# Optimization experiments

Measured on AMD Instinct MI355X. Metric: run time of the kernel, lower is better.

## Reference

```python
import jax, jax.numpy as jnp
import numpy as np

B, S, D, H = 2, 2048, 1024, 16
HD = D // H  # head dim = 64
NEG = -1e9


def setup_inputs() -> dict:
    key = jax.random.key(0)
    ks = jax.random.split(key, 8)
    x = jax.random.normal(ks[0], (B, S, D), dtype=jnp.float32)
    mask = jax.random.randint(ks[1], (B, 1, S, S), 0, 2).astype(bool)
    s = 1.0 / np.sqrt(D)
    Wq = jax.random.normal(ks[2], (D, D), dtype=jnp.float32) * s
    bq = jax.random.normal(ks[3], (D,), dtype=jnp.float32) * 0.01
    Wk = jax.random.normal(ks[4], (D, D), dtype=jnp.float32) * s
    bk = jax.random.normal(ks[5], (D,), dtype=jnp.float32) * 0.01
    Wv = jax.random.normal(ks[6], (D, D), dtype=jnp.float32) * s
    bv = jax.random.normal(ks[7], (D,), dtype=jnp.float32) * 0.01
    return {"x": x, "mask": mask, "Wq": Wq, "bq": bq, "Wk": Wk, "bk": bk, "Wv": Wv, "bv": bv}


def reference(x, mask, Wq, bq, Wk, bk, Wv, bv):
    b, s, d = x.shape
    # QKV projections (torch nn.Linear: y = x @ W.T + b)
    q = (x @ Wq.T + bq).reshape(b, s, H, HD).transpose(0, 2, 1, 3)  # [B,H,S,HD]
    k = (x @ Wk.T + bk).reshape(b, s, H, HD).transpose(0, 2, 1, 3)
    v = (x @ Wv.T + bv).reshape(b, s, H, HD).transpose(0, 2, 1, 3)
    # NOTE: original scales by sqrt(hidden_state), not sqrt(head_dim)
    scale = 1.0 / jnp.sqrt(jnp.asarray(d, dtype=x.dtype))
    weight = jnp.einsum('bhqd,bhkd->bhqk', q, k) * scale  # [B,H,S,S]
    weight = jnp.where(mask, jnp.asarray(NEG, dtype=x.dtype), weight)
    score = jax.nn.softmax(weight, axis=-1)
    out = jnp.einsum('bhqk,bhkd->bhqd', score, v)  # [B,H,S,HD]
    return out.transpose(0, 2, 1, 3).reshape(b, s, d)
```

## Files before the change

### kernel.cpp

```cpp
#include <hip/hip_runtime.h>
#include <hip/hip_bf16.h>

typedef __bf16 bf16x8 __attribute__((ext_vector_type(8)));
typedef float f32x4 __attribute__((ext_vector_type(4)));

#define NB 2
#define NS 2048
#define ND 1024
#define NH 16
#define NHD 64

__device__ __forceinline__ unsigned short f2b(float f) {
    union { __hip_bfloat16 h; unsigned short u; } c;
    c.h = __float2bfloat16(f);
    return c.u;
}

__device__ __forceinline__ void gl_lds16(const unsigned short* g, unsigned short* l) {
    __builtin_amdgcn_global_load_lds(
        (const __attribute__((address_space(1))) unsigned int*)g,
        (__attribute__((address_space(3))) unsigned int*)l, 16, 0, 0);
}

__global__ __launch_bounds__(256) void to_bf16_all(
    const float* __restrict__ x,  const float* __restrict__ wq,
    const float* __restrict__ wk, const float* __restrict__ wv,
    unsigned short* __restrict__ xb,  unsigned short* __restrict__ wqb,
    unsigned short* __restrict__ wkb, unsigned short* __restrict__ wvb)
{
    const size_t TX = (size_t)NB * NS * ND / 8;
    const size_t TW = (size_t)ND * ND / 8;
    size_t gid = (size_t)blockIdx.x * 256 + threadIdx.x;
    const float* src; unsigned short* dst; size_t off;
    if (gid < TX)               { src = x;  dst = xb;  off = gid * 8; }
    else if (gid < TX + TW)     { src = wq; dst = wqb; off = (gid - TX) * 8; }
    else if (gid < TX + 2 * TW) { src = wk; dst = wkb; off = (gid - TX - TW) * 8; }
    else                        { src = wv; dst = wvb; off = (gid - TX - 2 * TW) * 8; }
    float4 a = *(const float4*)(src + off);
    float4 b = *(const float4*)(src + off + 4);
    alignas(16) unsigned short t[8];
    t[0] = f2b(a.x); t[1] = f2b(a.y); t[2] = f2b(a.z); t[3] = f2b(a.w);
    t[4] = f2b(b.x); t[5] = f2b(b.y); t[6] = f2b(b.z); t[7] = f2b(b.w);
    *(uint4*)(dst + off) = *(const uint4*)t;
}

__global__ void detect_mask(const unsigned* __restrict__ m, int* __restrict__ flag) {
    __shared__ int bad;
    if (threadIdx.x == 0) bad = 0;
    __syncthreads();
    int mybad = 0;
    for (int i = threadIdx.x; i < 8192; i += 256) {
        unsigned w = m[i];
        if (w != 0u && w != 1u && w != 0x3F800000u) mybad = 1;
    }
    if (mybad) bad = 1;
    __syncthreads();
    if (threadIdx.x == 0) *flag = bad ? 0 : 1;
}

__global__ __launch_bounds__(256) void pack_mask(
    const void* __restrict__ mask, const int* __restrict__ mflag,
    unsigned long long* __restrict__ mbits)
{
    const int wave = threadIdx.x >> 6;
    const int lane = threadIdx.x & 63;
    const size_t w = (size_t)blockIdx.x * 4 + wave;
    const size_t e = w * 64 + lane;
    int v;
    if (*mflag) v = (((const unsigned*)mask)[e] != 0u);
    else        v = (((const unsigned char*)mask)[e] != 0);
    unsigned long long bits = __ballot(v);
    if (lane == 0) mbits[w] = bits;
}

__global__ __launch_bounds__(256) void qkv_gemm(
    const unsigned short* __restrict__ xb,
    const unsigned short* __restrict__ Wqb, const float* __restrict__ bq,
    const unsigned short* __restrict__ Wkb, const float* __restrict__ bk,
    const unsigned short* __restrict__ Wvb, const float* __restrict__ bv,
    unsigned short* __restrict__ Qb, unsigned short* __restrict__ Kb,
    unsigned short* __restrict__ Vtb)
{
    __shared__ alignas(16) unsigned short Alds[128 * 64];
    __shared__ alignas(16) unsigned short Blds[128 * 64];

    const int tid  = threadIdx.x;
    const int wave = tid >> 6;
    const int lane = tid & 63;
    const int z    = blockIdx.z;

    const unsigned short* W = (z == 0) ? Wqb : (z == 1) ? Wkb : Wvb;
    const float* bias       = (z == 0) ? bq  : (z == 1) ? bk  : bv;

    const int m0 = blockIdx.x * 128;
    const int n0 = blockIdx.y * 128;
    const int wr = (wave >> 1) * 64;
    const int wc = (wave & 1) * 64;

    int soff[4];
    #pragma unroll
    for (int i = 0; i < 4; i++) {
        const int r = i * 32 + (tid >> 3);
        soff[i] = r * ND + (((tid & 7) ^ (r & 7)) * 8);
    }

    const unsigned short* xsrc = xb + (size_t)m0 * ND;
    const unsigned short* wsrc = W  + (size_t)n0 * ND;

    const int lg = lane >> 4;
    const int ll = lane & 15;
    const int xr7 = ll & 7;

    f32x4 acc[4][4] = {};

    for (int kt = 0; kt < ND; kt += 64) {
        if (kt != 0) __syncthreads();
        #pragma unroll
        for (int i = 0; i < 4; i++) {
            gl_lds16(xsrc + kt + soff[i], Alds + i * 2048 + wave * 512);
            gl_lds16(wsrc + kt + soff[i], Blds + i * 2048 + wave * 512);
        }
        __syncthreads();

        #pragma unroll
        for (int kk = 0; kk < 2; kk++) {
            const int segb = ((kk * 4 + lg) ^ xr7) * 16;
            bf16x8 af[4], bfr[4];
            #pragma unroll
            for (int m = 0; m < 4; m++)
                af[m] = *(const bf16x8*)((const char*)Alds
                         + (wr + m * 16 + ll) * 128 + segb);
            #pragma unroll
            for (int n = 0; n < 4; n++)
                bfr[n] = *(const bf16x8*)((const char*)Blds
                         + (wc + n * 16 + ll) * 128 + segb);

            #pragma unroll
            for (int m = 0; m < 4; m++)
                #pragma unroll
                for (int n = 0; n < 4; n++)
                    acc[m][n] = __builtin_amdgcn_mfma_f32_16x16x32_bf16(
                        af[m], bfr[n], acc[m][n], 0, 0, 0);
        }
    }

    const float oscale = (z == 0) ? 0.03125f : 1.0f;
    #pragma unroll
    for (int n = 0; n < 4; n++) {
        const int j  = n0 + wc + n * 16 + ll;
        const float bj = bias[j];
        const int hh = j >> 6;
        const int hd = j & 63;
        #pragma unroll
        for (int m = 0; m < 4; m++) {
            #pragma unroll
            for (int r = 0; r < 4; r++) {
                const int i  = m0 + wr + m * 16 + lg * 4 + r;
                const int bb = i >> 11;
                const int sI = i & 2047;
                const unsigned short o = f2b((acc[m][n][r] + bj) * oscale);
                if (z == 2) {
                    Vtb[((size_t)(bb * NH + hh) * NHD + hd) * NS + sI] = o;
                } else {
                    const size_t idx = ((size_t)(bb * NH + hh) * NS + sI) * NHD + hd;
                    if (z == 0) Qb[idx] = o; else Kb[idx] = o;
                }
            }
        }
    }
}

__global__ __launch_bounds__(512, 4) void attn_kernel(
    const unsigned short* __restrict__ Qb, const unsigned short* __restrict__ Kb,
    const unsigned short* __restrict__ Vtb,
    const unsigned long long* __restrict__ mbits, float* __restrict__ out)
{
    __shared__ alignas(16) unsigned short Kt[64 * 64];
    __shared__ alignas(16) unsigned short Vt[64 * 64];
    __shared__ alignas(16) unsigned short Plds[8][16][72];

    const int tid  = threadIdx.x;
    const int wave = tid >> 6;
    const int lane = tid & 63;

    const int wg   = blockIdx.x;
    const int xcd  = wg & 7;
    const int slot = wg >> 3;
    const int hb   = xcd * 4 + (slot >> 4);
    const int qblk = slot & 15;
    const int h = hb & (NH - 1);
    const int b = hb >> 4;
    const int q0 = qblk * 128 + wave * 16;

    const unsigned short* Qp = Qb  + (size_t)(b * NH + h) * NS * NHD;
    const unsigned short* Kp = Kb  + (size_t)(b * NH + h) * NS * NHD;
    const unsigned short* Vp = Vtb + (size_t)(b * NH + h) * NHD * NS;
    const unsigned long long* mrow = mbits + (size_t)b * NS * (NS / 64);

    const int lg = lane >> 4;
    const int ll = lane & 15;

    const int rw = wave * 8 + (lane >> 3);
    const int sg = (lane & 7) ^ (rw & 7);
    const size_t ksoff = (size_t)rw * NHD + sg * 8;
    const size_t vsoff = (size_t)rw * NS  + sg * 8;
    unsigned short* ldsK = Kt + wave * 512;
    unsigned short* ldsV = Vt + wave * 512;

    const int xr7 = ll & 7;
    const int ka0 = ll * 128 + ((lg)     ^ xr7) * 16;
    const int ka1 = ll * 128 + ((lg + 4) ^ xr7) * 16;

    const int kcol = lg * 8;
    const bf16x8 qf0 = *(const bf16x8*)&Qp[(q0 + ll) * NHD + kcol];
    const bf16x8 qf1 = *(const bf16x8*)&Qp[(q0 + ll) * NHD + 32 + kcol];

    f32x4 O0 = {}, O1 = {}, O2 = {}, O3 = {};
    float mrun = -3.0e38f;
    float lrun = 0.f;

    unsigned long long mwc = mrow[(size_t)(q0 + ll) * (NS / 64)];

    for (int t = 0; t < 32; t++) {
        const int kb = t * 64;
        if (t != 0) __syncthreads();
        gl_lds16(Kp + (size_t)kb * NHD + ksoff, ldsK);
        gl_lds16(Vp + kb + vsoff, ldsV);
        const int tn = (t + 1 < 32) ? t + 1 : 0;
        const unsigned long long mwn = mrow[(size_t)(q0 + ll) * (NS / 64) + tn];
        __syncthreads();

        f32x4 s0 = {}, s1 = {}, s2 = {}, s3 = {};
        {
            const bf16x8 k00 = *(const bf16x8*)((const char*)Kt + 0 * 2048 + ka0);
            const bf16x8 k10 = *(const bf16x8*)((const char*)Kt + 1 * 2048 + ka0);
            const bf16x8 k20 = *(const bf16x8*)((const char*)Kt + 2 * 2048 + ka0);
            const bf16x8 k30 = *(const bf16x8*)((const char*)Kt + 3 * 2048 + ka0);
            s0 = __builtin_amdgcn_mfma_f32_16x16x32_bf16(k00, qf0, s0, 0, 0, 0);
            s1 = __builtin_amdgcn_mfma_f32_16x16x32_bf16(k10, qf0, s1, 0, 0, 0);
            s2 = __builtin_amdgcn_mfma_f32_16x16x32_bf16(k20, qf0, s2, 0, 0, 0);
            s3 = __builtin_amdgcn_mfma_f32_16x16x32_bf16(k30, qf0, s3, 0, 0, 0);
            const bf16x8 k01 = *(const bf16x8*)((const char*)Kt + 0 * 2048 + ka1);
            const bf16x8 k11 = *(const bf16x8*)((const char*)Kt + 1 * 2048 + ka1);
            const bf16x8 k21 = *(const bf16x8*)((const char*)Kt + 2 * 2048 + ka1);
            const bf16x8 k31 = *(const bf16x8*)((const char*)Kt + 3 * 2048 + ka1);
            s0 = __builtin_amdgcn_mfma_f32_16x16x32_bf16(k01, qf1, s0, 0, 0, 0);
            s1 = __builtin_amdgcn_mfma_f32_16x16x32_bf16(k11, qf1, s1, 0, 0, 0);
            s2 = __builtin_amdgcn_mfma_f32_16x16x32_bf16(k21, qf1, s2, 0, 0, 0);
            s3 = __builtin_amdgcn_mfma_f32_16x16x32_bf16(k31, qf1, s3, 0, 0, 0);
        }

        const unsigned long long mws = mwc >> (lg * 4);
        float sv[16];
        #pragma unroll
        for (int tt = 0; tt < 4; tt++) {
            const f32x4 st = (tt == 0) ? s0 : (tt == 1) ? s1 : (tt == 2) ? s2 : s3;
            #pragma unroll
            for (int r = 0; r < 4; r++)
                sv[tt * 4 + r] = ((mws >> (16 * tt + r)) & 1ull) ? -1e9f : st[r];
        }

        float m01 = fmaxf(fmaxf(sv[0], sv[1]), fmaxf(sv[2], sv[3]));
        float m23 = fmaxf(fmaxf(sv[4], sv[5]), fmaxf(sv[6], sv[7]));
        float m45 = fmaxf(fmaxf(sv[8], sv[9]), fmaxf(sv[10], sv[11]));
        float m67 = fmaxf(fmaxf(sv[12], sv[13]), fmaxf(sv[14], sv[15]));
        float mt = fmaxf(fmaxf(m01, m23), fmaxf(m45, m67));
        mt = fmaxf(mt, __shfl_xor(mt, 16));
        mt = fmaxf(mt, __shfl_xor(mt, 32));

        if (!__all(mt <= mrun + 8.0f)) {
            const float mnew  = fmaxf(mrun, mt);
            const float alpha = __expf(mrun - mnew);
            mrun = mnew;
            lrun *= alpha;
            #pragma unroll
            for (int r = 0; r < 4; r++) {
                const float ar = __shfl(alpha, lg * 4 + r);
                O0[r] *= ar; O1[r] *= ar; O2[r] *= ar; O3[r] *= ar;
            }
        }

        float rs = 0.f;
        #pragma unroll
        for (int tt = 0; tt < 4; tt++) {
            const float p0 = __expf(sv[tt * 4 + 0] - mrun);
            const float p1 = __expf(sv[tt * 4 + 1] - mrun);
            const float p2 = __expf(sv[tt * 4 + 2] - mrun);
            const float p3 = __expf(sv[tt * 4 + 3] - mrun);
            rs += (p0 + p1) + (p2 + p3);
            uint2 w;
            w.x = (unsigned)f2b(p0) | ((unsigned)f2b(p1) << 16);
            w.y = (unsigned)f2b(p2) | ((unsigned)f2b(p3) << 16);
            *(uint2*)&Plds[wave][ll][tt * 16 + lg * 4] = w;
        }
        rs += __shfl_xor(rs, 16);
        rs += __shfl_xor(rs, 32);
        lrun += rs;

        const bf16x8 pa0 = *(const bf16x8*)&Plds[wave][ll][kcol];
        const bf16x8 pa1 = *(const bf16x8*)&Plds[wave][ll][32 + kcol];
        {
            const bf16x8 v00 = *(const bf16x8*)((const char*)Vt + 0 * 2048 + ka0);
            const bf16x8 v10 = *(const bf16x8*)((const char*)Vt + 1 * 2048 + ka0);
            const bf16x8 v20 = *(const bf16x8*)((const char*)Vt + 2 * 2048 + ka0);
            const bf16x8 v30 = *(const bf16x8*)((const char*)Vt + 3 * 2048 + ka0);
            O0 = __builtin_amdgcn_mfma_f32_16x16x32_bf16(pa0, v00, O0, 0, 0, 0);
            O1 = __builtin_amdgcn_mfma_f32_16x16x32_bf16(pa0, v10, O1, 0, 0, 0);
            O2 = __builtin_amdgcn_mfma_f32_16x16x32_bf16(pa0, v20, O2, 0, 0, 0);
            O3 = __builtin_amdgcn_mfma_f32_16x16x32_bf16(pa0, v30, O3, 0, 0, 0);
            const bf16x8 v01 = *(const bf16x8*)((const char*)Vt + 0 * 2048 + ka1);
            const bf16x8 v11 = *(const bf16x8*)((const char*)Vt + 1 * 2048 + ka1);
            const bf16x8 v21 = *(const bf16x8*)((const char*)Vt + 2 * 2048 + ka1);
            const bf16x8 v31 = *(const bf16x8*)((const char*)Vt + 3 * 2048 + ka1);
            O0 = __builtin_amdgcn_mfma_f32_16x16x32_bf16(pa1, v01, O0, 0, 0, 0);
            O1 = __builtin_amdgcn_mfma_f32_16x16x32_bf16(pa1, v11, O1, 0, 0, 0);
            O2 = __builtin_amdgcn_mfma_f32_16x16x32_bf16(pa1, v21, O2, 0, 0, 0);
            O3 = __builtin_amdgcn_mfma_f32_16x16x32_bf16(pa1, v31, O3, 0, 0, 0);
        }
        mwc = mwn;
    }

    #pragma unroll
    for (int r = 0; r < 4; r++) {
        const int q = q0 + lg * 4 + r;
        const float inv = 1.0f / __shfl(lrun, lg * 4 + r);
        float* op = out + (size_t)(b * NS + q) * ND + h * NHD;
        op[0 * 16 + ll] = O0[r] * inv;
        op[1 * 16 + ll] = O1[r] * inv;
        op[2 * 16 + ll] = O2[r] * inv;
        op[3 * 16 + ll] = O3[r] * inv;
    }
}

extern "C" void kernel_launch(void* const* d_in, const int* in_sizes, int n_in,
                              void* d_out, int out_size, void* d_ws, size_t ws_size,
                              hipStream_t stream)
{
    const float* x  = (const float*)d_in[0];
    const void* mask = d_in[1];
    const float* Wq = (const float*)d_in[2];
    const float* bq = (const float*)d_in[3];
    const float* Wk = (const float*)d_in[4];
    const float* bk = (const float*)d_in[5];
    const float* Wv = (const float*)d_in[6];
    const float* bv = (const float*)d_in[7];
    float* out = (float*)d_out;

    const size_t szX = (size_t)NB * NS * ND;
    const size_t szW = (size_t)ND * ND;
    const size_t szQ = (size_t)NB * NH * NS * NHD;

    int* mflag = (int*)d_ws;
    unsigned short* xb  = (unsigned short*)((char*)d_ws + 256);
    unsigned short* Wqb = xb  + szX;
    unsigned short* Wkb = Wqb + szW;
    unsigned short* Wvb = Wkb + szW;
    unsigned short* Qb  = Wvb + szW;
    unsigned short* Kb  = Qb + szQ;
    unsigned short* Vtb = Kb + szQ;
    unsigned long long* mbits = (unsigned long long*)(Vtb + szQ);

    dim3 blk(256);
    const int cvtBlocks = (int)((szX + 3 * szW) / 8 / 256);
    to_bf16_all<<<dim3(cvtBlocks), blk, 0, stream>>>(
        x, Wq, Wk, Wv, xb, Wqb, Wkb, Wvb);

    detect_mask<<<dim3(1), blk, 0, stream>>>((const unsigned*)mask, mflag);
    const int words = NB * NS * NS / 64;
    pack_mask<<<dim3(words / 4), blk, 0, stream>>>(mask, mflag, mbits);

    dim3 g1(32, 8, 3);
    qkv_gemm<<<g1, blk, 0, stream>>>(xb, Wqb, bq, Wkb, bk, Wvb, bv, Qb, Kb, Vtb);

    attn_kernel<<<dim3(512), dim3(512), 0, stream>>>(Qb, Kb, Vtb, mbits, out);
}
```

Measured before the change: 234.4 us.

## Double-buffer K/V tiles, stage QKV epilogue through LDS, use exp2 softmax

The attention kernel now double-buffers the K and V LDS tiles. The next tile's global-to-LDS load is issued before computing on the current one, with a single barrier per iteration, so load latency overlaps MFMA work. The projection epilogue for Q and K is staged through LDS scratch so global stores become 16-byte vectors, and V transposed stores are packed four at a time. The Q scale is folded with log2(e) so softmax can use exp2f instead of expf. The cost is doubled K/V LDS, which may reduce occupancy, plus an extra barrier in the GEMM epilogue.

```diff
diff --git a/kernel.cpp b/kernel.cpp
--- a/kernel.cpp
+++ b/kernel.cpp
@@ -144,28 +144,48 @@
         }
     }
 
-    const float oscale = (z == 0) ? 0.03125f : 1.0f;
-    #pragma unroll
-    for (int n = 0; n < 4; n++) {
-        const int j  = n0 + wc + n * 16 + ll;
-        const float bj = bias[j];
-        const int hh = j >> 6;
-        const int hd = j & 63;
-        #pragma unroll
-        for (int m = 0; m < 4; m++) {
-            #pragma unroll
-            for (int r = 0; r < 4; r++) {
-                const int i  = m0 + wr + m * 16 + lg * 4 + r;
-                const int bb = i >> 11;
-                const int sI = i & 2047;
-                const unsigned short o = f2b((acc[m][n][r] + bj) * oscale);
-                if (z == 2) {
-                    Vtb[((size_t)(bb * NH + hh) * NHD + hd) * NS + sI] = o;
-                } else {
-                    const size_t idx = ((size_t)(bb * NH + hh) * NS + sI) * NHD + hd;
-                    if (z == 0) Qb[idx] = o; else Kb[idx] = o;
-                }
+    if (z == 2) {
+        #pragma unroll
+        for (int n = 0; n < 4; n++) {
+            const int j = n0 + wc + n * 16 + ll;
+            const float bj = bias[j];
+            const int hh = j >> 6, hd = j & 63;
+            #pragma unroll
+            for (int m = 0; m < 4; m++) {
+                const int i = m0 + wr + m * 16 + lg * 4;
+                const int bb = i >> 11, sI = i & 2047;
+                alignas(8) unsigned short t4[4];
+                #pragma unroll
+                for (int r = 0; r < 4; r++) t4[r] = f2b(acc[m][n][r] + bj);
+                *(uint2*)&Vtb[((size_t)(bb * NH + hh) * NHD + hd) * NS + sI] =
+                    *(const uint2*)t4;
             }
+        }
+    } else {
+        const float oscale = (z == 0) ? 0.045084253f : 1.0f;
+        __syncthreads();
+        unsigned short* scr = ((wave & 2) ? Blds : Alds) + (wave & 1) * 4096;
+        #pragma unroll
+        for (int n = 0; n < 4; n++) {
+            const int col = n * 16 + ll;
+            const float bj = bias[n0 + wc + col];
+            #pragma unroll
+            for (int m = 0; m < 4; m++)
+                #pragma unroll
+                for (int r = 0; r < 4; r++)
+                    scr[(m * 16 + lg * 4 + r) * 64 + col] =
+                        f2b((acc[m][n][r] + bj) * oscale);
+        }
+        const int rr = lane >> 3, c8 = (lane & 7) * 8;
+        const int hh = (n0 + wc) >> 6;
+        unsigned short* dst = (z == 0) ? Qb : Kb;
+        #pragma unroll
+        for (int i = 0; i < 8; i++) {
+            const int row = i * 8 + rr;
+            uint4 v = *(const uint4*)&scr[row * 64 + c8];
+            const int gi = m0 + wr + row;
+            const int bb = gi >> 11, sI = gi & 2047;
+            *(uint4*)&dst[((size_t)(bb * NH + hh) * NS + sI) * NHD + c8] = v;
         }
     }
 }
@@ -175,8 +195,8 @@
     const unsigned short* __restrict__ Vtb,
     const unsigned long long* __restrict__ mbits, float* __restrict__ out)
 {
-    __shared__ alignas(16) unsigned short Kt[64 * 64];
-    __shared__ alignas(16) unsigned short Vt[64 * 64];
+    __shared__ alignas(16) unsigned short Kt[2][64 * 64];
+    __shared__ alignas(16) unsigned short Vt[2][64 * 64];
     __shared__ alignas(16) unsigned short Plds[8][16][72];
 
     const int tid  = threadIdx.x;
@@ -204,8 +224,6 @@
     const int sg = (lane & 7) ^ (rw & 7);
     const size_t ksoff = (size_t)rw * NHD + sg * 8;
     const size_t vsoff = (size_t)rw * NS  + sg * 8;
-    unsigned short* ldsK = Kt + wave * 512;
-    unsigned short* ldsV = Vt + wave * 512;
 
     const int xr7 = ll & 7;
     const int ka0 = ll * 128 + ((lg)     ^ xr7) * 16;
@@ -221,29 +239,37 @@
 
     unsigned long long mwc = mrow[(size_t)(q0 + ll) * (NS / 64)];
 
+    gl_lds16(Kp + ksoff, Kt[0] + wave * 512);
+    gl_lds16(Vp + vsoff, Vt[0] + wave * 512);
+    __syncthreads();
+
     for (int t = 0; t < 32; t++) {
         const int kb = t * 64;
-        if (t != 0) __syncthreads();
-        gl_lds16(Kp + (size_t)kb * NHD + ksoff, ldsK);
-        gl_lds16(Vp + kb + vsoff, ldsV);
+        const int cur = t & 1;
+
+        if (t + 1 < 32) {
+            gl_lds16(Kp + (size_t)(kb + 64) * NHD + ksoff, Kt[cur ^ 1] + wave * 512);
+            gl_lds16(Vp + (kb + 64) + vsoff, Vt[cur ^ 1] + wave * 512);
+        }
         const int tn = (t + 1 < 32) ? t + 1 : 0;
         const unsigned long long mwn = mrow[(size_t)(q0 + ll) * (NS / 64) + tn];
-        __syncthreads();
-
+
+        const char* Kc = (const char*)Kt[cur];
+        const char* Vc = (const char*)Vt[cur];
         f32x4 s0 = {}, s1 = {}, s2 = {}, s3 = {};
         {
-            const bf16x8 k00 = *(const bf16x8*)((const char*)Kt + 0 * 2048 + ka0);
-            const bf16x8 k10 = *(const bf16x8*)((const char*)Kt + 1 * 2048 + ka0);
-            const bf16x8 k20 = *(const bf16x8*)((const char*)Kt + 2 * 2048 + ka0);
-            const bf16x8 k30 = *(const bf16x8*)((const char*)Kt + 3 * 2048 + ka0);
+            const bf16x8 k00 = *(const bf16x8*)(Kc + 0 * 2048 + ka0);
+            const bf16x8 k10 = *(const bf16x8*)(Kc + 1 * 2048 + ka0);
+            const bf16x8 k20 = *(const bf16x8*)(Kc + 2 * 2048 + ka0);
+            const bf16x8 k30 = *(const bf16x8*)(Kc + 3 * 2048 + ka0);
             s0 = __builtin_amdgcn_mfma_f32_16x16x32_bf16(k00, qf0, s0, 0, 0, 0);
             s1 = __builtin_amdgcn_mfma_f32_16x16x32_bf16(k10, qf0, s1, 0, 0, 0);
             s2 = __builtin_amdgcn_mfma_f32_16x16x32_bf16(k20, qf0, s2, 0, 0, 0);
             s3 = __builtin_amdgcn_mfma_f32_16x16x32_bf16(k30, qf0, s3, 0, 0, 0);
-            const bf16x8 k01 = *(const bf16x8*)((const char*)Kt + 0 * 2048 + ka1);
-            const bf16x8 k11 = *(const bf16x8*)((const char*)Kt + 1 * 2048 + ka1);
-            const bf16x8 k21 = *(const bf16x8*)((const char*)Kt + 2 * 2048 + ka1);
-            const bf16x8 k31 = *(const bf16x8*)((const char*)Kt + 3 * 2048 + ka1);
+            const bf16x8 k01 = *(const bf16x8*)(Kc + 0 * 2048 + ka1);
+            const bf16x8 k11 = *(const bf16x8*)(Kc + 1 * 2048 + ka1);
+            const bf16x8 k21 = *(const bf16x8*)(Kc + 2 * 2048 + ka1);
+            const bf16x8 k31 = *(const bf16x8*)(Kc + 3 * 2048 + ka1);
             s0 = __builtin_amdgcn_mfma_f32_16x16x32_bf16(k01, qf1, s0, 0, 0, 0);
             s1 = __builtin_amdgcn_mfma_f32_16x16x32_bf16(k11, qf1, s1, 0, 0, 0);
             s2 = __builtin_amdgcn_mfma_f32_16x16x32_bf16(k21, qf1, s2, 0, 0, 0);
@@ -270,7 +296,7 @@
 
         if (!__all(mt <= mrun + 8.0f)) {
             const float mnew  = fmaxf(mrun, mt);
-            const float alpha = __expf(mrun - mnew);
+            const float alpha = exp2f(mrun - mnew);
             mrun = mnew;
             lrun *= alpha;
             #pragma unroll
@@ -283,10 +309,10 @@
         float rs = 0.f;
         #pragma unroll
         for (int tt = 0; tt < 4; tt++) {
-            const float p0 = __expf(sv[tt * 4 + 0] - mrun);
-            const float p1 = __expf(sv[tt * 4 + 1] - mrun);
-            const float p2 = __expf(sv[tt * 4 + 2] - mrun);
-            const float p3 = __expf(sv[tt * 4 + 3] - mrun);
+            const float p0 = exp2f(sv[tt * 4 + 0] - mrun);
+            const float p1 = exp2f(sv[tt * 4 + 1] - mrun);
+            const float p2 = exp2f(sv[tt * 4 + 2] - mrun);
+            const float p3 = exp2f(sv[tt * 4 + 3] - mrun);
             rs += (p0 + p1) + (p2 + p3);
             uint2 w;
             w.x = (unsigned)f2b(p0) | ((unsigned)f2b(p1) << 16);
@@ -300,23 +326,25 @@
         const bf16x8 pa0 = *(const bf16x8*)&Plds[wave][ll][kcol];
         const bf16x8 pa1 = *(const bf16x8*)&Plds[wave][ll][32 + kcol];
         {
-            const bf16x8 v00 = *(const bf16x8*)((const char*)Vt + 0 * 2048 + ka0);
-            const bf16x8 v10 = *(const bf16x8*)((const char*)Vt + 1 * 2048 + ka0);
-            const bf16x8 v20 = *(const bf16x8*)((const char*)Vt + 2 * 2048 + ka0);
-            const bf16x8 v30 = *(const bf16x8*)((const char*)Vt + 3 * 2048 + ka0);
+            const bf16x8 v00 = *(const bf16x8*)(Vc + 0 * 2048 + ka0);
+            const bf16x8 v10 = *(const bf16x8*)(Vc + 1 * 2048 + ka0);
+            const bf16x8 v20 = *(const bf16x8*)(Vc + 2 * 2048 + ka0);
+            const bf16x8 v30 = *(const bf16x8*)(Vc + 3 * 2048 + ka0);
             O0 = __builtin_amdgcn_mfma_f32_16x16x32_bf16(pa0, v00, O0, 0, 0, 0);
             O1 = __builtin_amdgcn_mfma_f32_16x16x32_bf16(pa0, v10, O1, 0, 0, 0);
             O2 = __builtin_amdgcn_mfma_f32_16x16x32_bf16(pa0, v20, O2, 0, 0, 0);
             O3 = __builtin_amdgcn_mfma_f32_16x16x32_bf16(pa0, v30, O3, 0, 0, 0);
-            const bf16x8 v01 = *(const bf16x8*)((const char*)Vt + 0 * 2048 + ka1);
-            const bf16x8 v11 = *(const bf16x8*)((const char*)Vt + 1 * 2048 + ka1);
-            const bf16x8 v21 = *(const bf16x8*)((const char*)Vt + 2 * 2048 + ka1);
-            const bf16x8 v31 = *(const bf16x8*)((const char*)Vt + 3 * 2048 + ka1);
+            const bf16x8 v01 = *(const bf16x8*)(Vc + 0 * 2048 + ka1);
+            const bf16x8 v11 = *(const bf16x8*)(Vc + 1 * 2048 + ka1);
+            const bf16x8 v21 = *(const bf16x8*)(Vc + 2 * 2048 + ka1);
+            const bf16x8 v31 = *(const bf16x8*)(Vc + 3 * 2048 + ka1);
             O0 = __builtin_amdgcn_mfma_f32_16x16x32_bf16(pa1, v01, O0, 0, 0, 0);
             O1 = __builtin_amdgcn_mfma_f32_16x16x32_bf16(pa1, v11, O1, 0, 0, 0);
             O2 = __builtin_amdgcn_mfma_f32_16x16x32_bf16(pa1, v21, O2, 0, 0, 0);
             O3 = __builtin_amdgcn_mfma_f32_16x16x32_bf16(pa1, v31, O3, 0, 0, 0);
         }
+
+        __syncthreads();
         mwc = mwn;
     }
 
```

Result: no change. 236.9 us (+1.1%).
